# Kernel optimization log

Hardware: AMD Instinct MI355X
Metric: run time of the kernel (lower is better)

The kernel has to match this reference:

```python
import jax, jax.numpy as jnp
import numpy as np

D_MODEL = 768
N_HEAD = 12
N_KV_HEADS = 4
HEAD_DIM = D_MODEL // N_HEAD
N_REPEAT = N_HEAD // N_KV_HEADS
ROPE_BASE = 10000.0


def _rotate_half(x):
    # Faithful to the torch impl: reshape(..., 2, d/2) -> transpose(-2,-1) -> reshape
    # (interleaves the two halves), then chunk and cat(-x2, x1).
    d = x.shape[-1]
    xh = x.reshape(*x.shape[:-1], 2, d // 2).swapaxes(-2, -1).reshape(x.shape)
    x1, x2 = jnp.split(xh, 2, axis=-1)
    return jnp.concatenate([-x2, x1], axis=-1)


def _rope(x, pos):
    # x: [B, h, T, d], pos: [T] int
    d = x.shape[-1]
    inv_freq = 1.0 / (ROPE_BASE ** (jnp.arange(0, d, 2, dtype=jnp.float32) / d))
    freqs = pos.astype(jnp.float32)[:, None] * inv_freq[None, :]      # [T, d/2]
    emb = jnp.concatenate([freqs, freqs], axis=-1)                     # [T, d]
    cos = jnp.cos(emb)[None, None]                                     # [1,1,T,d]
    sin = jnp.sin(emb)[None, None]
    xf = x.astype(jnp.float32)
    return (xf * cos + _rotate_half(xf) * sin).astype(x.dtype)


def setup_inputs() -> dict:
    key = jax.random.key(0)
    ks = jax.random.split(key, 6)
    B, T, C = 8, 1024, D_MODEL
    s = 0.02
    return {
        "x": jax.random.normal(ks[0], (B, T, C), dtype=jnp.float32),
        "pos": jnp.arange(T, dtype=jnp.int32),
        "q_w": jax.random.normal(ks[1], (C, N_HEAD * HEAD_DIM), dtype=jnp.float32) * s,
        "q_b": jnp.zeros((N_HEAD * HEAD_DIM,), dtype=jnp.float32),
        "k_w": jax.random.normal(ks[2], (C, N_KV_HEADS * HEAD_DIM), dtype=jnp.float32) * s,
        "k_b": jnp.zeros((N_KV_HEADS * HEAD_DIM,), dtype=jnp.float32),
        "v_w": jax.random.normal(ks[3], (C, N_KV_HEADS * HEAD_DIM), dtype=jnp.float32) * s,
        "v_b": jnp.zeros((N_KV_HEADS * HEAD_DIM,), dtype=jnp.float32),
        "o_w": jax.random.normal(ks[4], (C, C), dtype=jnp.float32) * s,
        "o_b": jnp.zeros((C,), dtype=jnp.float32),
    }


def reference(x, pos, q_w, q_b, k_w, k_b, v_w, v_b, o_w, o_b):
    B, T, C = x.shape
    hd, H, KVH, rep = HEAD_DIM, N_HEAD, N_KV_HEADS, N_REPEAT

    Q = (x @ q_w + q_b).reshape(B, T, H, hd).transpose(0, 2, 1, 3)     # [B,H,T,hd]
    K = (x @ k_w + k_b).reshape(B, T, KVH, hd).transpose(0, 2, 1, 3)   # [B,KVH,T,hd]
    V = (x @ v_w + v_b).reshape(B, T, KVH, hd).transpose(0, 2, 1, 3)

    Q = _rope(Q, pos)
    K = _rope(K, pos)

    # Grouped attention: avoid materializing repeated KV (equiv. to repeat_interleave).
    Qg = Q.reshape(B, KVH, rep, T, hd)
    scores = jnp.einsum("bgrtd,bgsd->bgrts", Qg, K) / np.sqrt(hd).astype(np.float32)
    causal = jnp.tril(jnp.ones((T, T), dtype=bool))
    scores = jnp.where(causal, scores, jnp.finfo(scores.dtype).min)
    probs = jax.nn.softmax(scores, axis=-1)
    out = jnp.einsum("bgrts,bgsd->bgrtd", probs, V)                    # [B,KVH,rep,T,hd]
    out = out.reshape(B, H, T, hd).transpose(0, 2, 1, 3).reshape(B, T, C)
    return out @ o_w + o_b
```

## Files before the change

### kernel.cpp

```cpp
#include <hip/hip_runtime.h>
#include <hip/hip_bf16.h>
#include <math.h>

#define BATCH 8
#define SEQ   1024
#define DM    768
#define NHEAD 12
#define KVH   4
#define HD    64
#define REP   3

#define QSCALE 0.18033688011112042f
#define ROPE_C (13.287712379549449f / 32.0f)

typedef unsigned short u16;
typedef __attribute__((ext_vector_type(8))) __bf16 bf16x8;
typedef __attribute__((ext_vector_type(4))) float f32x4;
typedef __attribute__((ext_vector_type(4))) unsigned int u32x4;
typedef __attribute__((address_space(1))) const unsigned int gu32_c;
typedef __attribute__((address_space(3))) unsigned int su32;

__device__ __forceinline__ u16 f2bf(float f) {
    unsigned int u = __float_as_uint(f);
    u += 0x7fffu + ((u >> 16) & 1u);
    return (u16)(u >> 16);
}

__global__ __launch_bounds__(256) void cvt_all(
    const float* __restrict__ x,
    const float* __restrict__ qw, const float* __restrict__ kw,
    const float* __restrict__ vw, const float* __restrict__ ow,
    u16* __restrict__ xb, u16* __restrict__ wqkvt, u16* __restrict__ wot)
{
    const int NX = 8192 * DM / 4;
    const int NW = 1280 * DM;
    const int NO = DM * DM;
    const int i = blockIdx.x * 256 + threadIdx.x;
    if (i < NX) {
        const float4 v = ((const float4*)x)[i];
        ushort4 r;
        r.x = f2bf(v.x); r.y = f2bf(v.y); r.z = f2bf(v.z); r.w = f2bf(v.w);
        ((ushort4*)xb)[i] = r;
    } else if (i < NX + NW) {
        const int idx = i - NX;
        const int k = idx % DM;
        const int n = idx / DM;
        float v;
        if (n < 768)       v = qw[(size_t)k * 768 + n] * QSCALE;
        else if (n < 1024) v = kw[(size_t)k * 256 + (n - 768)];
        else               v = vw[(size_t)k * 256 + (n - 1024)];
        wqkvt[idx] = f2bf(v);
    } else if (i < NX + NW + NO) {
        const int idx = i - NX - NW;
        const int k = idx % DM;
        const int n = idx / DM;
        wot[idx] = f2bf(ow[(size_t)k * DM + n]);
    }
}

__device__ __forceinline__ void gemm64_body(
    const u16* __restrict__ A, const u16* __restrict__ B,
    int m0, int n0, u16 (*As)[2048], u16 (*Bs)[4096], f32x4 acc[2][4])
{
    const int tid  = threadIdx.x;
    const int lane = tid & 63;
    const int wid  = tid >> 6;
    const int wr = wid >> 1, wc = wid & 1;
    const int lo = lane & 15, hi = lane >> 4;

    const f32x4 z = {0.f, 0.f, 0.f, 0.f};
    #pragma unroll
    for (int i = 0; i < 2; i++)
        #pragma unroll
        for (int j = 0; j < 4; j++)
            acc[i][j] = z;

    const int NT = DM / 32;
    const int rowA = tid >> 2;
    const int colA = (tid & 3) << 3;

    #define STAGE_G(kt_, sl_) do {                                            \
        __builtin_amdgcn_global_load_lds(                                     \
            (gu32_c*)&A[(size_t)(m0 + rowA) * DM + (kt_) * 32 + colA],        \
            (su32*)&As[sl_][wid << 9], 16, 0, 0);                             \
        _Pragma("unroll")                                                     \
        for (int r_ = 0; r_ < 2; ++r_) {                                      \
            const int idx_  = r_ * 256 + tid;                                 \
            const int row_  = idx_ >> 2;                                      \
            const int col_  = (idx_ & 3) << 3;                                \
            const int base_ = (r_ * 256 + wid * 64) * 8;                      \
            __builtin_amdgcn_global_load_lds(                                 \
                (gu32_c*)&B[(size_t)(n0 + row_) * DM + (kt_) * 32 + col_],    \
                (su32*)&Bs[sl_][base_], 16, 0, 0);                            \
        }                                                                     \
    } while (0)

    STAGE_G(0, 0);
    STAGE_G(1, 1);

    for (int kt = 0; kt < NT; ++kt) {
        const int k2 = (kt + 2 < NT) ? kt + 2 : NT - 1;
        STAGE_G(k2, (kt + 2) & 3);
        asm volatile("s_waitcnt vmcnt(6)" ::: "memory");
        __builtin_amdgcn_s_barrier();
        __builtin_amdgcn_sched_barrier(0);

        const int sl = kt & 3;
        bf16x8 af[2], bfr[4];
        #pragma unroll
        for (int i = 0; i < 2; i++) af[i]  = *(const bf16x8*)&As[sl][(wr * 32 + i * 16 + lo) * 32 + hi * 8];
        #pragma unroll
        for (int j = 0; j < 4; j++) bfr[j] = *(const bf16x8*)&Bs[sl][(wc * 64 + j * 16 + lo) * 32 + hi * 8];
        #pragma unroll
        for (int i = 0; i < 2; i++)
            #pragma unroll
            for (int j = 0; j < 4; j++)
                acc[i][j] = __builtin_amdgcn_mfma_f32_16x16x32_bf16(af[i], bfr[j], acc[i][j], 0, 0, 0);
    }
    #undef STAGE_G
}

__global__ __launch_bounds__(256, 2) void gemm_qkv(
    const u16* __restrict__ xb, const u16* __restrict__ wt,
    const float* __restrict__ qb, const float* __restrict__ kb,
    const float* __restrict__ vb, const int* __restrict__ pos,
    u16* __restrict__ Q, u16* __restrict__ K, u16* __restrict__ Vt)
{
    __shared__ __align__(16) u16 As[4][2048];
    __shared__ __align__(16) u16 Bs[4][4096];
    const int id = (blockIdx.x & 7) * 160 + (blockIdx.x >> 3);
    const int m0 = (id / 10) * 64;
    const int n0 = (id % 10) * 128;
    f32x4 acc[2][4];
    gemm64_body(xb, wt, m0, n0, As, Bs, acc);

    const int tid = threadIdx.x;
    const int lane = tid & 63, wid = tid >> 6;
    const int wr = wid >> 1, wc = wid & 1;
    const int lo = lane & 15, hi = lane >> 4;

    const int seg = n0 + wc * 64;

    if (seg >= 1024) {
        #pragma unroll
        for (int j = 0; j < 4; j++) {
            const int nl = seg - 1024 + j * 16 + lo;
            const float bias = vb[nl];
            const int head = nl >> 6, d = nl & 63;
            #pragma unroll
            for (int i = 0; i < 2; i++) {
                ushort4 vs;
                vs.x = f2bf(acc[i][j][0] + bias);
                vs.y = f2bf(acc[i][j][1] + bias);
                vs.z = f2bf(acc[i][j][2] + bias);
                vs.w = f2bf(acc[i][j][3] + bias);
                const int m = m0 + wr * 32 + i * 16 + hi * 4;
                const int b = m >> 10, t = m & 1023;
                *(ushort4*)&Vt[(((size_t)(b * KVH + head)) * HD + d) * SEQ + t] = vs;
            }
        }
    } else {
        const bool isQ = seg < 768;
        const int  segl = isQ ? seg : seg - 768;
        const int  head = segl >> 6;
        const int  Hcnt = isQ ? NHEAD : KVH;
        u16* outp = isQ ? Q : K;
        float bias[4];
        #pragma unroll
        for (int j = 0; j < 4; j++) {
            const int nl = segl + j * 16 + lo;
            bias[j] = isQ ? qb[nl] * QSCALE : kb[nl];
        }
        const float inv0 = exp2f(-(float)lo * ROPE_C);
        const float inv1 = exp2f(-(float)(16 + lo) * ROPE_C);
        int pmode;
        if (pos[1] == 1)                         pmode = 0;
        else if (((const float*)pos)[1] == 1.0f) pmode = 1;
        else                                     pmode = 2;
        const int src0 = (hi << 4) | (lo >> 1);
        const int src1 = src0 | 8;
        const bool odd = (lo & 1) != 0;

        #pragma unroll
        for (int i = 0; i < 2; i++) {
            #pragma unroll
            for (int r = 0; r < 4; r++) {
                const float v0 = acc[i][0][r] + bias[0];
                const float v1 = acc[i][1][r] + bias[1];
                const float v2 = acc[i][2][r] + bias[2];
                const float v3 = acc[i][3][r] + bias[3];
                const float p0e = __shfl(v1, src0), p0o = __shfl(v3, src0);
                const float p1e = __shfl(v1, src1), p1o = __shfl(v3, src1);
                const float p2e = __shfl(v0, src0), p2o = __shfl(v2, src0);
                const float p3e = __shfl(v0, src1), p3o = __shfl(v2, src1);
                const float px0 = odd ? p0o : p0e;
                const float px1 = odd ? p1o : p1e;
                const float px2 = odd ? p2o : p2e;
                const float px3 = odd ? p3o : p3e;

                const int m = m0 + wr * 32 + i * 16 + hi * 4 + r;
                const int b = m >> 10, t = m & 1023;
                float pp;
                if (pmode == 0)      pp = (float)pos[t];
                else if (pmode == 1) pp = ((const float*)pos)[t];
                else                 pp = (float)pos[2 * t];

                float sv0, cv0, sv1, cv1;
                sincosf(pp * inv0, &sv0, &cv0);
                sincosf(pp * inv1, &sv1, &cv1);
                const float o0 = v0 * cv0 - px0 * sv0;
                const float o1 = v1 * cv1 - px1 * sv1;
                const float o2 = v2 * cv0 + px2 * sv0;
                const float o3 = v3 * cv1 + px3 * sv1;

                u16* dst = outp + ((size_t)(b * Hcnt + head) * SEQ + t) * HD;
                dst[lo]      = f2bf(o0);
                dst[16 + lo] = f2bf(o1);
                dst[32 + lo] = f2bf(o2);
                dst[48 + lo] = f2bf(o3);
            }
        }
    }
}

__global__ __launch_bounds__(256, 2) void gemm_oproj(
    const u16* __restrict__ Ab, const u16* __restrict__ wt,
    const float* __restrict__ ob, float* __restrict__ outp)
{
    __shared__ __align__(16) u16 As[4][2048];
    __shared__ __align__(16) u16 Bs[4][4096];
    const int id = (blockIdx.x & 7) * 96 + (blockIdx.x >> 3);
    const int m0 = (id / 6) * 64;
    const int n0 = (id % 6) * 128;
    f32x4 acc[2][4];
    gemm64_body(Ab, wt, m0, n0, As, Bs, acc);

    const int tid = threadIdx.x;
    const int lane = tid & 63, wid = tid >> 6;
    const int wr = wid >> 1, wc = wid & 1;
    const int lo = lane & 15, hi = lane >> 4;

    #pragma unroll
    for (int j = 0; j < 4; j++) {
        const int n = n0 + wc * 64 + j * 16 + lo;
        const float bias = ob[n];
        #pragma unroll
        for (int i = 0; i < 2; i++) {
            #pragma unroll
            for (int r = 0; r < 4; r++) {
                const int m = m0 + wr * 32 + i * 16 + hi * 4 + r;
                outp[(size_t)m * DM + n] = acc[i][j][r] + bias;
            }
        }
    }
}

__device__ __forceinline__ void strip_compute(
    const bf16x8& qf0, const bf16x8& qf1,
    const bf16x8& k0, const bf16x8& k1, const bf16x8& k2, const bf16x8& k3,
    const bf16x8* vv, bool diag, int msk0, int hi,
    float& m, float& l, f32x4* O)
{
    const f32x4 z = {0.f, 0.f, 0.f, 0.f};
    f32x4 a0 = z, a1 = z;
    __builtin_amdgcn_s_setprio(1);
    a0 = __builtin_amdgcn_mfma_f32_16x16x32_bf16(k0, qf0, a0, 0, 0, 0);
    a0 = __builtin_amdgcn_mfma_f32_16x16x32_bf16(k1, qf1, a0, 0, 0, 0);
    a1 = __builtin_amdgcn_mfma_f32_16x16x32_bf16(k2, qf0, a1, 0, 0, 0);
    a1 = __builtin_amdgcn_mfma_f32_16x16x32_bf16(k3, qf1, a1, 0, 0, 0);
    __builtin_amdgcn_s_setprio(0);

    float sc[8];
    #pragma unroll
    for (int e = 0; e < 8; ++e)
        sc[e] = (e < 4) ? a0[e & 3] : a1[e & 3];
    if (diag) {
        #pragma unroll
        for (int e = 0; e < 8; ++e) {
            const int srel = ((e >> 2) << 4) + (hi << 2) + (e & 3);
            if (srel > msk0) sc[e] = -3.0e38f;
        }
    }
    float pm = sc[0];
    #pragma unroll
    for (int e = 1; e < 8; ++e) pm = fmaxf(pm, sc[e]);

    if (!__all(pm - m <= 8.0f)) {
        float pr = fmaxf(pm, __shfl_xor(pm, 16));
        pr = fmaxf(pr, __shfl_xor(pr, 32));
        const float mn = fmaxf(m, pr);
        const float f = exp2f(m - mn);
        l *= f;
        #pragma unroll
        for (int r = 0; r < 4; ++r) {
            const float fr = __shfl(f, hi * 4 + r);
            #pragma unroll
            for (int dj = 0; dj < 4; ++dj) O[dj][r] *= fr;
        }
        m = mn;
    }

    union { u16 u[8]; bf16x8 v; } pu;
    float ps = 0.f;
    #pragma unroll
    for (int e = 0; e < 8; ++e) {
        const float p = exp2f(sc[e] - m);
        ps += p;
        pu.u[e] = f2bf(p);
    }
    l += ps;

    __builtin_amdgcn_s_setprio(1);
    #pragma unroll
    for (int dj = 0; dj < 4; ++dj)
        O[dj] = __builtin_amdgcn_mfma_f32_16x16x32_bf16(pu.v, vv[dj], O[dj], 0, 0, 0);
    __builtin_amdgcn_s_setprio(0);
}

__global__ __launch_bounds__(256, 4) void attn_mfma(
    const u16* __restrict__ Q, const u16* __restrict__ K,
    const u16* __restrict__ Vt, u16* __restrict__ outp)
{
    __shared__ __align__(16) u16 Ks[4][2048];
    __shared__ __align__(16) u16 Vs[4][2048];

    const int blk = blockIdx.x;
    const int xcd = blk & 7;
    const int jj  = blk >> 3;
    const int bg  = (xcd << 2) + (jj & 3);
    const int rh  = jj >> 2;
    const int a   = 15 - rh / 3;
    const int hl  = rh % 3;
    const int b   = bg >> 2, g = bg & 3;
    const int h   = g * REP + hl;

    const int wid  = threadIdx.x >> 6;
    const int lane = threadIdx.x & 63;
    const int lo = lane & 15, hi = lane >> 4;

    const int w    = (a << 2) + wid;
    const int q0   = w << 4;
    const int dT   = w >> 1;
    const int msk0 = lo + ((w & 1) << 4);
    const int nstT = (a << 1) + 2;

    const u16* Kp = K  + (size_t)(b * KVH + g) * SEQ * HD;
    const u16* Vp = Vt + (size_t)(b * KVH + g) * SEQ * HD;

    const int jK = (wid << 6) + lane;
    const int sKoff = (jK ^ ((jK >> 3) & 7)) << 3;
    int vsoff[4];
    #pragma unroll
    for (int q = 0; q < 4; ++q) {
        const int dw  = (wid << 8) + (q << 6) + lane;
        const int R   = dw >> 4;
        const int wd  = dw & 15;
        const int hpl = (wd >> 2) ^ ((R >> 1) & 3);
        vsoff[q] = (R << 10) + (hpl << 2) + (((wd >> 1) & 1) << 4) + ((wd & 1) << 1);
    }

    const u16* Qp = Q + ((size_t)(b * NHEAD + h) * SEQ + q0) * HD;
    const bf16x8 qf0 = *(const bf16x8*)&Qp[(size_t)lo * HD + hi * 8];
    const bf16x8 qf1 = *(const bf16x8*)&Qp[(size_t)lo * HD + 32 + hi * 8];

    const f32x4 z = {0.f, 0.f, 0.f, 0.f};
    f32x4 O[4];
    #pragma unroll
    for (int dj = 0; dj < 4; ++dj) O[dj] = z;
    float m = -3.0e38f, l = 0.f;

    #define STAGE(st_, sl_) do {                                              \
        const int s0_ = (st_) << 5;                                           \
        __builtin_amdgcn_global_load_lds(                                     \
            (gu32_c*)(Kp + (s0_ << 6) + sKoff),                               \
            (su32*)&Ks[sl_][wid << 9], 16, 0, 0);                             \
        _Pragma("unroll")                                                     \
        for (int q_ = 0; q_ < 4; ++q_)                                        \
            __builtin_amdgcn_global_load_lds(                                 \
                (gu32_c*)(Vp + s0_ + vsoff[q_]),                              \
                (su32*)&Vs[sl_][(wid << 9) + (q_ << 7)], 4, 0, 0);            \
    } while (0)

    STAGE(0, 0);
    STAGE(1, 1);

    const int xorK = lo & 7;
    for (int st = 0; st < nstT; ++st) {
        const int s2 = (st + 2 < nstT) ? st + 2 : nstT - 1;
        STAGE(s2, (st + 2) & 3);
        asm volatile("s_waitcnt vmcnt(10)" ::: "memory");
        __builtin_amdgcn_s_barrier();
        __builtin_amdgcn_sched_barrier(0);

        if (st <= dT) {
            const int sl = st & 3;
            const u16* kb_ = Ks[sl];
            const bf16x8 k0 = *(const bf16x8*)&kb_[((lo << 3) + (hi ^ xorK)) << 3];
            const bf16x8 k1 = *(const bf16x8*)&kb_[((lo << 3) + ((4 + hi) ^ xorK)) << 3];
            const bf16x8 k2 = *(const bf16x8*)&kb_[(((16 + lo) << 3) + (hi ^ xorK)) << 3];
            const bf16x8 k3 = *(const bf16x8*)&kb_[(((16 + lo) << 3) + ((4 + hi) ^ xorK)) << 3];
            bf16x8 vv[4];
            #pragma unroll
            for (int dj = 0; dj < 4; ++dj) {
                const int R = dj * 16 + lo;
                vv[dj] = *(const bf16x8*)&Vs[sl][(R << 5) + ((hi ^ ((R >> 1) & 3)) << 3)];
            }
            strip_compute(qf0, qf1, k0, k1, k2, k3, vv, st == dT, msk0, hi, m, l, O);
        }
    }
    #undef STAGE

    l += __shfl_xor(l, 16); l += __shfl_xor(l, 32);
    #pragma unroll
    for (int r = 0; r < 4; ++r) {
        const float li = 1.0f / fmaxf(__shfl(l, hi * 4 + r), 1e-37f);
        const int t = q0 + hi * 4 + r;
        #pragma unroll
        for (int dj = 0; dj < 4; ++dj)
            outp[((size_t)(b * SEQ + t)) * DM + h * HD + dj * 16 + lo] = f2bf(O[dj][r] * li);
    }
}

extern "C" void kernel_launch(void* const* d_in, const int* in_sizes, int n_in,
                              void* d_out, int out_size, void* d_ws, size_t ws_size,
                              hipStream_t stream) {
    const float* x   = (const float*)d_in[0];
    const int*   pos = (const int*)d_in[1];
    const float* qw  = (const float*)d_in[2];
    const float* qb  = (const float*)d_in[3];
    const float* kw  = (const float*)d_in[4];
    const float* kb  = (const float*)d_in[5];
    const float* vw  = (const float*)d_in[6];
    const float* vb  = (const float*)d_in[7];
    const float* ow  = (const float*)d_in[8];
    const float* ob  = (const float*)d_in[9];
    float* out = (float*)d_out;

    u16* xb    = (u16*)d_ws;
    u16* Wqkvt = xb    + (size_t)8192 * DM;
    u16* Wot   = Wqkvt + (size_t)1280 * DM;
    u16* Qbuf  = Wot   + (size_t)DM * DM;
    u16* Kbuf  = Qbuf  + (size_t)BATCH * NHEAD * SEQ * HD;
    u16* Vtb   = Kbuf  + (size_t)BATCH * KVH * SEQ * HD;
    u16* attn  = xb;

    const int NCVT = 8192 * DM / 4 + 1280 * DM + DM * DM;
    cvt_all<<<(NCVT + 255) / 256, 256, 0, stream>>>(x, qw, kw, vw, ow, xb, Wqkvt, Wot);

    gemm_qkv<<<1280, 256, 0, stream>>>(xb, Wqkvt, qb, kb, vb, pos, Qbuf, Kbuf, Vtb);

    attn_mfma<<<1536, 256, 0, stream>>>(Qbuf, Kbuf, Vtb, attn);

    gemm_oproj<<<768, 256, 0, stream>>>(attn, Wot, ob, out);
}
```

Before: 196.3 us.

## Process two 16-row query strips per wave in attention, halving block count

Each attention wave now handles 32 query rows as two 16-row strips that share the same K/V fragments loaded from LDS, so each block covers 128 query rows and the grid shrinks from 1536 to 768 blocks. This halves K/V staging traffic per query row and doubles the MFMA work done per LDS read. The cost is more accumulator registers, which is why launch bounds drop from 4 to 3 blocks per CU, along with coarser causal load balance. Separately, the RoPE sincosf calls in the QKV GEMM are replaced with the fast __sinf/__cosf intrinsics, which lose accuracy for large angles.

```diff
diff --git a/kernel.cpp b/kernel.cpp
--- a/kernel.cpp
+++ b/kernel.cpp
@@ -205,9 +205,9 @@
                 else if (pmode == 1) pp = ((const float*)pos)[t];
                 else                 pp = (float)pos[2 * t];
 
-                float sv0, cv0, sv1, cv1;
-                sincosf(pp * inv0, &sv0, &cv0);
-                sincosf(pp * inv1, &sv1, &cv1);
+                const float a0 = pp * inv0, a1 = pp * inv1;
+                const float sv0 = __sinf(a0), cv0 = __cosf(a0);
+                const float sv1 = __sinf(a1), cv1 = __cosf(a1);
                 const float o0 = v0 * cv0 - px0 * sv0;
                 const float o1 = v1 * cv1 - px1 * sv1;
                 const float o2 = v2 * cv0 + px2 * sv0;
@@ -317,7 +317,7 @@
     __builtin_amdgcn_s_setprio(0);
 }
 
-__global__ __launch_bounds__(256, 4) void attn_mfma(
+__global__ __launch_bounds__(256, 3) void attn_mfma(
     const u16* __restrict__ Q, const u16* __restrict__ K,
     const u16* __restrict__ Vt, u16* __restrict__ outp)
 {
@@ -329,7 +329,7 @@
     const int jj  = blk >> 3;
     const int bg  = (xcd << 2) + (jj & 3);
     const int rh  = jj >> 2;
-    const int a   = 15 - rh / 3;
+    const int a   = 7 - rh / 3;
     const int hl  = rh % 3;
     const int b   = bg >> 2, g = bg & 3;
     const int h   = g * REP + hl;
@@ -338,11 +338,12 @@
     const int lane = threadIdx.x & 63;
     const int lo = lane & 15, hi = lane >> 4;
 
-    const int w    = (a << 2) + wid;
-    const int q0   = w << 4;
-    const int dT   = w >> 1;
-    const int msk0 = lo + ((w & 1) << 4);
-    const int nstT = (a << 1) + 2;
+    const int w0   = (a << 3) + (wid << 1);
+    const int q0   = w0 << 4;
+    const int dT   = (a << 2) + wid;
+    const int mskA = lo;
+    const int mskB = 16 + lo;
+    const int nstT = (a << 2) + 4;
 
     const u16* Kp = K  + (size_t)(b * KVH + g) * SEQ * HD;
     const u16* Vp = Vt + (size_t)(b * KVH + g) * SEQ * HD;
@@ -359,15 +360,18 @@
         vsoff[q] = (R << 10) + (hpl << 2) + (((wd >> 1) & 1) << 4) + ((wd & 1) << 1);
     }
 
-    const u16* Qp = Q + ((size_t)(b * NHEAD + h) * SEQ + q0) * HD;
-    const bf16x8 qf0 = *(const bf16x8*)&Qp[(size_t)lo * HD + hi * 8];
-    const bf16x8 qf1 = *(const bf16x8*)&Qp[(size_t)lo * HD + 32 + hi * 8];
+    const u16* QpA = Q + ((size_t)(b * NHEAD + h) * SEQ + q0) * HD;
+    const u16* QpB = QpA + (size_t)16 * HD;
+    const bf16x8 qA0 = *(const bf16x8*)&QpA[(size_t)lo * HD + hi * 8];
+    const bf16x8 qA1 = *(const bf16x8*)&QpA[(size_t)lo * HD + 32 + hi * 8];
+    const bf16x8 qB0 = *(const bf16x8*)&QpB[(size_t)lo * HD + hi * 8];
+    const bf16x8 qB1 = *(const bf16x8*)&QpB[(size_t)lo * HD + 32 + hi * 8];
 
     const f32x4 z = {0.f, 0.f, 0.f, 0.f};
-    f32x4 O[4];
-    #pragma unroll
-    for (int dj = 0; dj < 4; ++dj) O[dj] = z;
-    float m = -3.0e38f, l = 0.f;
+    f32x4 OA[4], OB[4];
+    #pragma unroll
+    for (int dj = 0; dj < 4; ++dj) { OA[dj] = z; OB[dj] = z; }
+    float mA = -3.0e38f, lA = 0.f, mB = -3.0e38f, lB = 0.f;
 
     #define STAGE(st_, sl_) do {                                              \
         const int s0_ = (st_) << 5;                                           \
@@ -405,19 +409,26 @@
                 const int R = dj * 16 + lo;
                 vv[dj] = *(const bf16x8*)&Vs[sl][(R << 5) + ((hi ^ ((R >> 1) & 3)) << 3)];
             }
-            strip_compute(qf0, qf1, k0, k1, k2, k3, vv, st == dT, msk0, hi, m, l, O);
+            const bool diag = (st == dT);
+            strip_compute(qA0, qA1, k0, k1, k2, k3, vv, diag, mskA, hi, mA, lA, OA);
+            strip_compute(qB0, qB1, k0, k1, k2, k3, vv, diag, mskB, hi, mB, lB, OB);
         }
     }
     #undef STAGE
 
-    l += __shfl_xor(l, 16); l += __shfl_xor(l, 32);
+    lA += __shfl_xor(lA, 16); lA += __shfl_xor(lA, 32);
+    lB += __shfl_xor(lB, 16); lB += __shfl_xor(lB, 32);
     #pragma unroll
     for (int r = 0; r < 4; ++r) {
-        const float li = 1.0f / fmaxf(__shfl(l, hi * 4 + r), 1e-37f);
-        const int t = q0 + hi * 4 + r;
-        #pragma unroll
-        for (int dj = 0; dj < 4; ++dj)
-            outp[((size_t)(b * SEQ + t)) * DM + h * HD + dj * 16 + lo] = f2bf(O[dj][r] * li);
+        const float liA = 1.0f / fmaxf(__shfl(lA, hi * 4 + r), 1e-37f);
+        const float liB = 1.0f / fmaxf(__shfl(lB, hi * 4 + r), 1e-37f);
+        const int tA = q0 + hi * 4 + r;
+        const int tB = tA + 16;
+        #pragma unroll
+        for (int dj = 0; dj < 4; ++dj) {
+            outp[((size_t)(b * SEQ + tA)) * DM + h * HD + dj * 16 + lo] = f2bf(OA[dj][r] * liA);
+            outp[((size_t)(b * SEQ + tB)) * DM + h * HD + dj * 16 + lo] = f2bf(OB[dj][r] * liB);
+        }
     }
 }
 
@@ -449,7 +460,7 @@
 
     gemm_qkv<<<1280, 256, 0, stream>>>(xb, Wqkvt, qb, kb, vb, pos, Qbuf, Kbuf, Vtb);
 
-    attn_mfma<<<1536, 256, 0, stream>>>(Qbuf, Kbuf, Vtb, attn);
+    attn_mfma<<<768, 256, 0, stream>>>(Qbuf, Kbuf, Vtb, attn);
 
     gemm_oproj<<<768, 256, 0, stream>>>(attn, Wot, ob, out);
 }
```

After: 194.8 us. No clear change (-0.7%).
